# Kernel tuning notes

Measured on AMD Instinct MI355X. Metric: run time of the kernel, lower is better.

Reference implementation:

```python
import jax, jax.numpy as jnp
import numpy as np

B, N, H, F = 4, 4096, 128, 64
ADJ_DENSITY = 0.01


def setup_inputs() -> dict:
    key = jax.random.key(0)
    k1, k2, k3, k4, k5 = jax.random.split(key, 5)
    x = jax.random.normal(k1, (B, N, H), dtype=jnp.float32)
    w_scale = jnp.float32(1.0 / np.sqrt(H))  # ~ nn.Linear init scale
    Wq = jax.random.normal(k2, (H, F), dtype=jnp.float32) * w_scale
    Wk = jax.random.normal(k3, (H, F), dtype=jnp.float32) * w_scale
    Wv = jax.random.normal(k4, (H, F), dtype=jnp.float32) * w_scale
    # Sparse binary adjacency with self-loops (every row has >=1 neighbor,
    # so no all--inf softmax rows).
    adj = (jax.random.uniform(k5, (N, N)) < ADJ_DENSITY).astype(jnp.float32)
    diag = jnp.arange(N)
    adj = adj.at[diag, diag].set(1.0)
    return {"x": x, "Wq": Wq, "Wk": Wk, "Wv": Wv, "adj": adj}


def reference(x, Wq, Wk, Wv, adj):
    # x: (B,N,H); Wq/Wk/Wv: (H,F); adj: (N,N) binary, broadcast over batch.
    q = x @ Wq  # (B,N,F)
    k = x @ Wk  # (B,N,F)
    v = x @ Wv  # (B,N,F)
    scale = jnp.float32(F) ** -0.5  # k.shape[-1] ** -0.5
    scores = jnp.einsum("bnf,bmf->bnm", q, k) * scale  # (B,N,N)
    scores = jnp.where(adj[None] == 0, -jnp.inf, scores)
    # softmax over neighbors, then the module adds the adjacency back (wei + adj)
    wei = jax.nn.softmax(scores, axis=-1) + adj[None]  # (B,N,N)
    # dropout is identity in eval/deterministic reference
    out = jnp.einsum("bnm,bmf->bnf", wei, v)  # (B,N,F)
    return out
```

## Files before the change

### kernel.cpp

```cpp
#include <hip/hip_runtime.h>
#include <math.h>

#define Bb 4
#define Nn 4096
#define Hh 128
#define Ff 64
#define CAP 128

typedef __attribute__((ext_vector_type(8))) short bf16x8;
typedef __attribute__((ext_vector_type(4))) float f32x4;

__device__ __forceinline__ unsigned short f2bf(float f) {
  unsigned int u = __float_as_uint(f);
  u += 0x7fffu + ((u >> 16) & 1u);
  return (unsigned short)(u >> 16);
}
__device__ __forceinline__ float bf2f(unsigned short h) {
  return __uint_as_float(((unsigned int)h) << 16);
}

__global__ __launch_bounds__(256) void prep2_kernel(
    const float* __restrict__ x,
    const float* __restrict__ Wq,
    const float* __restrict__ Wk,
    const float* __restrict__ Wv,
    const float* __restrict__ adj,
    float* __restrict__ q,
    unsigned short* __restrict__ kb,
    unsigned short* __restrict__ vb,
    unsigned long long* __restrict__ bm) {
  __shared__ short xs[16 * 128];

  const int tid = threadIdx.x;
  const int w = tid >> 6;
  const int lane = tid & 63;
  const int bid = (int)blockIdx.x;

  if (bid < 1024) {
    const int row0 = bid * 16;
    const int half = lane >> 4;
    const int l16 = lane & 15;

    const float4* xg = (const float4*)(x + (size_t)row0 * Hh);
#pragma unroll
    for (int j = 0; j < 2; ++j) {
      const int idx = tid + 256 * j;
      const int row = idx >> 5;
      const int c4 = idx & 31;
      const float4 xv = xg[idx];
      uint2 p;
      p.x = (unsigned)f2bf(xv.x) | ((unsigned)f2bf(xv.y) << 16);
      p.y = (unsigned)f2bf(xv.z) | ((unsigned)f2bf(xv.w) << 16);
      const int addr = (row * 256 + c4 * 8) ^ ((row & 7) << 4);
      *(uint2*)((char*)xs + addr) = p;
    }

    bf16x8 bfr[3][4];
#pragma unroll
    for (int nt = 0; nt < 3; ++nt) {
      const int n0g = w * 48 + nt * 16;
      const float* Wm = (n0g < 64) ? Wq : (n0g < 128) ? Wk : Wv;
      const int c0 = n0g & 63;
#pragma unroll
      for (int ks = 0; ks < 4; ++ks) {
        bf16x8 f;
#pragma unroll
        for (int j = 0; j < 8; ++j) {
          const int kr = ks * 32 + half * 8 + j;
          f[j] = (short)f2bf(Wm[kr * Ff + c0 + l16]);
        }
        bfr[nt][ks] = f;
      }
    }
    __syncthreads();

    f32x4 acc[3];
#pragma unroll
    for (int nt = 0; nt < 3; ++nt)
#pragma unroll
      for (int r = 0; r < 4; ++r) acc[nt][r] = 0.f;

#pragma unroll
    for (int ks = 0; ks < 4; ++ks) {
      const int addr = (l16 * 256 + ks * 64 + half * 16) ^ ((l16 & 7) << 4);
      const bf16x8 a = *(const bf16x8*)((const char*)xs + addr);
#pragma unroll
      for (int nt = 0; nt < 3; ++nt) {
        acc[nt] = __builtin_amdgcn_mfma_f32_16x16x32_bf16(a, bfr[nt][ks],
                                                          acc[nt], 0, 0, 0);
      }
    }

#pragma unroll
    for (int nt = 0; nt < 3; ++nt) {
      const int n0g = w * 48 + nt * 16;
      const int col = (n0g & 63) + l16;
#pragma unroll
      for (int r = 0; r < 4; ++r) {
        const size_t rowg = (size_t)row0 + half * 4 + r;
        const float val = acc[nt][r];
        if (n0g < 64)
          q[rowg * Ff + col] = val;
        else if (n0g < 128)
          kb[rowg * Ff + col] = f2bf(val);
        else
          vb[rowg * Ff + col] = f2bf(val);
      }
    }
  } else {
    const int sid = bid - 1024;
    const int wg = sid * 4 + w;
    const float4* base = ((const float4*)adj) + ((size_t)wg * 8) * 64 + lane;

    float4 a[8];
#pragma unroll
    for (int it = 0; it < 8; ++it) a[it] = base[it * 64];

#pragma unroll
    for (int it = 0; it < 8; ++it) {
      const unsigned long long b0 = __ballot(a[it].x != 0.f);
      const unsigned long long b1 = __ballot(a[it].y != 0.f);
      const unsigned long long b2 = __ballot(a[it].z != 0.f);
      const unsigned long long b3 = __ballot(a[it].w != 0.f);
      const unsigned long long bsel =
          lane == 0 ? b0 : lane == 1 ? b1 : lane == 2 ? b2 : b3;
      if (lane < 4) bm[((size_t)wg * 8 + it) * 4 + lane] = bsel;
    }
  }
}

__global__ __launch_bounds__(256) void attn_kernel(
    const unsigned long long* __restrict__ bm,
    const float* __restrict__ q,
    const unsigned short* __restrict__ kb,
    const unsigned short* __restrict__ vb,
    float* __restrict__ out) {
  __shared__ __align__(8) unsigned short nbr[CAP];
  __shared__ float qs[4][64];
  __shared__ float ps[4][64];
  __shared__ int s_tot;

  const int n = blockIdx.x;
  const int tid = threadIdx.x;
  const int w = tid >> 6;
  const int lane = tid & 63;

  qs[w][lane] = q[((size_t)w * Nn + n) * Ff + lane];

  if (w == 0) {
    unsigned long long m = bm[(size_t)n * 64 + lane];
    const int cnt = __popcll(m);
    int inc = cnt;
#pragma unroll
    for (int o = 1; o < 64; o <<= 1) {
      const int t = __shfl_up(inc, o, 64);
      if (lane >= o) inc += t;
    }
    int pos = inc - cnt;
    const int colbase = ((lane >> 2) << 8) + (lane & 3);
    while (m) {
      const int i = __builtin_ctzll(m);
      if (pos < CAP) nbr[pos] = (unsigned short)(colbase + (i << 2));
      ++pos;
      m &= m - 1;
    }
    if (lane == 63) s_tot = inc;
  }
  __syncthreads();

  const int tot = s_tot < CAP ? s_tot : CAP;

  const int b = w;
  const unsigned short* kbb = kb + (size_t)b * Nn * Ff;
  const unsigned short* vbb = vb + (size_t)b * Nn * Ff;

  const int g = lane >> 2;
  const int sl = lane & 3;

  float4 q0a = *(const float4*)&qs[b][8 * sl];
  float4 q0b = *(const float4*)&qs[b][8 * sl + 4];
  float4 q1a = *(const float4*)&qs[b][32 + 8 * sl];
  float4 q1b = *(const float4*)&qs[b][32 + 8 * sl + 4];

  float M = -INFINITY, L = 0.f, acc = 0.f, vsum = 0.f;

  const int ntiles = (tot + 63) >> 6;
  for (int t = 0; t < ntiles; ++t) {
    const int tbase = t << 6;

    float s0, s1, s2, s3;
#define BPAIR(u, qlo, qhi, a)                                   \
    {                                                           \
      const float flo = __uint_as_float((u) << 16);             \
      const float fhi = __uint_as_float((u) & 0xffff0000u);     \
      a = fmaf(qlo, flo, a);                                    \
      a = fmaf(qhi, fhi, a);                                    \
    }
#define DOT_ROW(i, sdst)                                                  \
    {                                                                     \
      const int idx = tbase + g + 16 * (i);                               \
      const bool valid = idx < tot;                                       \
      const int m = valid ? (int)nbr[idx] : 0;                            \
      const char* krow = (const char*)(kbb + (size_t)m * Ff);             \
      const uint4 k0 = *(const uint4*)(krow + 16 * sl);                   \
      const uint4 k1 = *(const uint4*)(krow + 64 + 16 * sl);              \
      float a = 0.f;                                                      \
      BPAIR(k0.x, q0a.x, q0a.y, a)                                        \
      BPAIR(k0.y, q0a.z, q0a.w, a)                                        \
      BPAIR(k0.z, q0b.x, q0b.y, a)                                        \
      BPAIR(k0.w, q0b.z, q0b.w, a)                                        \
      BPAIR(k1.x, q1a.x, q1a.y, a)                                        \
      BPAIR(k1.y, q1a.z, q1a.w, a)                                        \
      BPAIR(k1.z, q1b.x, q1b.y, a)                                        \
      BPAIR(k1.w, q1b.z, q1b.w, a)                                        \
      a += __shfl_xor(a, 1, 64);                                          \
      a += __shfl_xor(a, 2, 64);                                          \
      sdst = valid ? a * 0.125f : -INFINITY;                              \
    }
    DOT_ROW(0, s0)
    DOT_ROW(1, s1)
    DOT_ROW(2, s2)
    DOT_ROW(3, s3)
#undef DOT_ROW
#undef BPAIR

    float lm = fmaxf(fmaxf(s0, s1), fmaxf(s2, s3));
#pragma unroll
    for (int o = 32; o; o >>= 1) lm = fmaxf(lm, __shfl_xor(lm, o, 64));
    const float newM = fmaxf(M, lm);

    const float p0 = (s0 == -INFINITY) ? 0.f : __expf(s0 - newM);
    const float p1 = (s1 == -INFINITY) ? 0.f : __expf(s1 - newM);
    const float p2 = (s2 == -INFINITY) ? 0.f : __expf(s2 - newM);
    const float p3 = (s3 == -INFINITY) ? 0.f : __expf(s3 - newM);

    float psum = ((p0 + p1) + (p2 + p3));
#pragma unroll
    for (int o = 32; o >= 4; o >>= 1) psum += __shfl_xor(psum, o, 64);

    const float corr = __expf(M - newM);
    L = L * corr + psum;
    acc *= corr;
    M = newM;

    const float pw = sl == 0 ? p0 : sl == 1 ? p1 : sl == 2 ? p2 : p3;
    ps[w][g + 16 * sl] = pw;

    const int jmax = min(64, tot - tbase);
#pragma unroll 4
    for (int j = 0; j < jmax; ++j) {
      const int m = nbr[tbase + j];
      const float vf = bf2f(vbb[(size_t)m * Ff + lane]);
      acc = fmaf(ps[w][j], vf, acc);
      vsum += vf;
    }
  }

  out[((size_t)b * Nn + n) * Ff + lane] = acc / L + vsum;
}

extern "C" void kernel_launch(void* const* d_in, const int* in_sizes, int n_in,
                              void* d_out, int out_size, void* d_ws, size_t ws_size,
                              hipStream_t stream) {
  const float* x = (const float*)d_in[0];
  const float* Wq = (const float*)d_in[1];
  const float* Wk = (const float*)d_in[2];
  const float* Wv = (const float*)d_in[3];
  const float* adj = (const float*)d_in[4];
  float* out = (float*)d_out;

  char* ws = (char*)d_ws;
  const size_t rows = (size_t)Bb * Nn;
  float* q = (float*)ws;
  unsigned short* kb = (unsigned short*)(ws + rows * Ff * 4);
  unsigned short* vb = (unsigned short*)(ws + rows * Ff * 4 + rows * Ff * 2);
  unsigned long long* bm = (unsigned long long*)(ws + rows * Ff * 8);

  prep2_kernel<<<dim3(3072), dim3(256), 0, stream>>>(
      x, Wq, Wk, Wv, adj, q, kb, vb, bm);
  attn_kernel<<<dim3(Nn), dim3(256), 0, stream>>>(bm, q, kb, vb, out);
}
```

Before: 47.88 us.

## Peel first neighbor tile and prefetch all K/V rows into registers

The first 64-neighbor tile is peeled out of the loop. All of its K row loads and all 64 V gathers are issued up front into registers, so the scattered global loads overlap instead of being serialized inside the per-neighbor accumulate loop. The neighbor list is zero-filled so padding indices are safe to load, and padded entries are masked out of the V sum. The max reduction also drops the redundant intra-group shuffles. The cost is heavy register use (64 V values per lane), which may lower occupancy.

```diff
diff --git a/kernel.cpp b/kernel.cpp
--- a/kernel.cpp
+++ b/kernel.cpp
@@ -148,6 +148,7 @@
   qs[w][lane] = q[((size_t)w * Nn + n) * Ff + lane];
 
   if (w == 0) {
+    ((ushort2*)nbr)[lane] = make_ushort2(0, 0);
     unsigned long long m = bm[(size_t)n * 64 + lane];
     const int cnt = __popcll(m);
     int inc = cnt;
@@ -184,18 +185,88 @@
 
   float M = -INFINITY, L = 0.f, acc = 0.f, vsum = 0.f;
 
+#define BPAIR(u, qlo, qhi, a)                                   \
+  {                                                             \
+    const float flo = __uint_as_float((u) << 16);               \
+    const float fhi = __uint_as_float((u) & 0xffff0000u);       \
+    a = fmaf(qlo, flo, a);                                      \
+    a = fmaf(qhi, fhi, a);                                      \
+  }
+
+  {
+    bool vld[4];
+    uint4 hk0[4], hk1[4];
+#pragma unroll
+    for (int i = 0; i < 4; ++i) {
+      const int idx = g + 16 * i;
+      vld[i] = idx < tot;
+      const int m = vld[i] ? (int)nbr[idx] : 0;
+      const char* krow = (const char*)(kbb + (size_t)m * Ff);
+      hk0[i] = *(const uint4*)(krow + 16 * sl);
+      hk1[i] = *(const uint4*)(krow + 64 + 16 * sl);
+    }
+
+    unsigned vreg[64];
+#pragma unroll
+    for (int j = 0; j < 64; ++j) {
+      vreg[j] = vbb[(size_t)nbr[j] * Ff + lane];
+    }
+
+    float s0, s1, s2, s3;
+#define SCORE(i, sdst)                                                  \
+    {                                                                   \
+      float a = 0.f;                                                    \
+      BPAIR(hk0[i].x, q0a.x, q0a.y, a)                                  \
+      BPAIR(hk0[i].y, q0a.z, q0a.w, a)                                  \
+      BPAIR(hk0[i].z, q0b.x, q0b.y, a)                                  \
+      BPAIR(hk0[i].w, q0b.z, q0b.w, a)                                  \
+      BPAIR(hk1[i].x, q1a.x, q1a.y, a)                                  \
+      BPAIR(hk1[i].y, q1a.z, q1a.w, a)                                  \
+      BPAIR(hk1[i].z, q1b.x, q1b.y, a)                                  \
+      BPAIR(hk1[i].w, q1b.z, q1b.w, a)                                  \
+      a += __shfl_xor(a, 1, 64);                                        \
+      a += __shfl_xor(a, 2, 64);                                        \
+      sdst = vld[i] ? a * 0.125f : -INFINITY;                           \
+    }
+    SCORE(0, s0)
+    SCORE(1, s1)
+    SCORE(2, s2)
+    SCORE(3, s3)
+#undef SCORE
+
+    float lm = fmaxf(fmaxf(s0, s1), fmaxf(s2, s3));
+#pragma unroll
+    for (int o = 32; o >= 4; o >>= 1) lm = fmaxf(lm, __shfl_xor(lm, o, 64));
+    const float newM = fmaxf(M, lm);
+
+    const float p0 = (s0 == -INFINITY) ? 0.f : __expf(s0 - newM);
+    const float p1 = (s1 == -INFINITY) ? 0.f : __expf(s1 - newM);
+    const float p2 = (s2 == -INFINITY) ? 0.f : __expf(s2 - newM);
+    const float p3 = (s3 == -INFINITY) ? 0.f : __expf(s3 - newM);
+
+    float psum = ((p0 + p1) + (p2 + p3));
+#pragma unroll
+    for (int o = 32; o >= 4; o >>= 1) psum += __shfl_xor(psum, o, 64);
+
+    L = psum;
+    M = newM;
+
+    const float pw = sl == 0 ? p0 : sl == 1 ? p1 : sl == 2 ? p2 : p3;
+    ps[w][g + 16 * sl] = pw;
+
+#pragma unroll
+    for (int j = 0; j < 64; ++j) {
+      const float vf = __uint_as_float(vreg[j] << 16);
+      acc = fmaf(ps[w][j], vf, acc);
+      vsum += (j < tot) ? vf : 0.f;
+    }
+  }
+
   const int ntiles = (tot + 63) >> 6;
-  for (int t = 0; t < ntiles; ++t) {
+  for (int t = 1; t < ntiles; ++t) {
     const int tbase = t << 6;
 
     float s0, s1, s2, s3;
-#define BPAIR(u, qlo, qhi, a)                                   \
-    {                                                           \
-      const float flo = __uint_as_float((u) << 16);             \
-      const float fhi = __uint_as_float((u) & 0xffff0000u);     \
-      a = fmaf(qlo, flo, a);                                    \
-      a = fmaf(qhi, fhi, a);                                    \
-    }
 #define DOT_ROW(i, sdst)                                                  \
     {                                                                     \
       const int idx = tbase + g + 16 * (i);                               \
@@ -222,11 +293,10 @@
     DOT_ROW(2, s2)
     DOT_ROW(3, s3)
 #undef DOT_ROW
-#undef BPAIR
 
     float lm = fmaxf(fmaxf(s0, s1), fmaxf(s2, s3));
 #pragma unroll
-    for (int o = 32; o; o >>= 1) lm = fmaxf(lm, __shfl_xor(lm, o, 64));
+    for (int o = 32; o >= 4; o >>= 1) lm = fmaxf(lm, __shfl_xor(lm, o, 64));
     const float newM = fmaxf(M, lm);
 
     const float p0 = (s0 == -INFINITY) ? 0.f : __expf(s0 - newM);
@@ -255,6 +325,7 @@
       vsum += vf;
     }
   }
+#undef BPAIR
 
   out[((size_t)b * Nn + n) * Ff + lane] = acc / L + vsum;
 }
```

Result: slower. 49.83 us (+4.1%).
